# Optimization experiments

Measured on AMD Instinct MI355X. Metric: run time of the kernel, lower is better.

## Reference

```python
import jax, jax.numpy as jnp
import numpy as np

H = 256          # h_dim
SEQ_LEN = 10     # max history length
B = 2048         # number of queries with non-empty history
N = 327680       # total flattened neighbors across all (query, timestep) segments
NUM_SEG = B * SEQ_LEN
NUM_ENT = 20000
NUM_REL = 200


def setup_inputs() -> dict:
    key = jax.random.key(0)
    ks = jax.random.split(key, 9)
    s = jax.random.randint(ks[0], (B,), 0, NUM_ENT)
    r = jax.random.randint(ks[1], (B,), 0, NUM_REL)
    nbr_ids = jax.random.randint(ks[2], (N,), 0, NUM_ENT)
    seg_ids = jnp.sort(jax.random.randint(ks[3], (N,), 0, NUM_SEG))
    ent_embeds = jax.random.normal(ks[4], (NUM_ENT, H), dtype=jnp.float32)
    rel_embeds = jax.random.normal(ks[5], (NUM_REL, H), dtype=jnp.float32)
    W_attn = jax.random.normal(ks[6], (3 * H, H), dtype=jnp.float32) * 0.05
    b_attn = jax.random.normal(ks[7], (H,), dtype=jnp.float32) * 0.05
    v_s = jax.random.normal(ks[8], (H, 1), dtype=jnp.float32) * 0.05
    return {"s": s, "r": r, "nbr_ids": nbr_ids, "seg_ids": seg_ids,
            "ent_embeds": ent_embeds, "rel_embeds": rel_embeds,
            "W_attn": W_attn, "b_attn": b_attn, "v_s": v_s}


def reference(s, r, nbr_ids, seg_ids, ent_embeds, rel_embeds, W_attn, b_attn, v_s):
    # Per-neighbor gathers. Each neighbor belongs to segment seg = q*SEQ_LEN + t.
    q = seg_ids // SEQ_LEN                              # query index per neighbor [N]
    em = ent_embeds[nbr_ids]                            # [N, H] neighbor embeddings
    s_emb = ent_embeds[s]                               # [B, H]
    r_emb = rel_embeds[r]                               # [B, H]
    ss = s_emb[q]                                       # [N, H]
    rr = r_emb[q]                                       # [N, H]
    # Score: tanh(Linear(3H -> H)) @ v_s  -> scalar per neighbor
    x = jnp.concatenate([em, ss, rr], axis=1)           # [N, 3H]
    scores = (jnp.tanh(x @ W_attn + b_attn) @ v_s)[:, 0]  # [N]
    # Segment softmax over neighbors within each (query, timestep) segment.
    m = jax.ops.segment_max(scores, seg_ids, num_segments=NUM_SEG)  # [S]
    e = jnp.exp(scores - m[seg_ids])                    # [N]
    denom = jax.ops.segment_sum(e, seg_ids, num_segments=NUM_SEG)   # [S]
    w = e / denom[seg_ids]                              # [N]
    # Weighted sum of neighbor embeddings per segment (scatter-reduce).
    agg = jax.ops.segment_sum(w[:, None] * em, seg_ids, num_segments=NUM_SEG)  # [S, H]
    counts = jax.ops.segment_sum(jnp.ones_like(scores), seg_ids, num_segments=NUM_SEG)
    mask = (counts > 0).astype(em.dtype).reshape(B, SEQ_LEN, 1)     # present timesteps
    agg = agg.reshape(B, SEQ_LEN, H)
    ss_t = jnp.broadcast_to(s_emb[:, None, :], (B, SEQ_LEN, H))
    rr_t = jnp.broadcast_to(r_emb[:, None, :], (B, SEQ_LEN, H))
    # Padded [B, SEQ_LEN, 3H] sequence tensor (rows for empty segments are zero,
    # matching the torch code's zero-initialized padded tensor). Dropout p=0.0.
    out = jnp.concatenate([agg, ss_t, rr_t], axis=2) * mask
    return out
```

## Files before the change

kernel.cpp:

```cpp
#include <hip/hip_runtime.h>
#include <hip/hip_bf16.h>

#define H 256
#define SEQ 10
#define C2LOG2E 2.8853900817779268f
#define LOG2E 1.4426950408889634f

typedef __attribute__((ext_vector_type(8))) short bf16x8;
typedef __attribute__((ext_vector_type(4))) float f32x4;

__device__ __forceinline__ unsigned short f2bf(float x) {
    union { float f; unsigned u; } v; v.f = x;
    unsigned r = v.u + 0x7fff + ((v.u >> 16) & 1);
    return (unsigned short)(r >> 16);
}
__device__ __forceinline__ float bf2f(unsigned short b) {
    union { unsigned u; float f; } v; v.u = ((unsigned)b) << 16;
    return v.f;
}
__device__ __forceinline__ float fexp2(float x) {
    return __builtin_amdgcn_exp2f(x);
}

__global__ void prep_kernel(const float* __restrict__ W,
                            unsigned short* __restrict__ Wt,
                            const int* __restrict__ seg_ids,
                            int* __restrict__ seg_start,
                            int nWt, int n, int num_seg) {
    if ((int)blockIdx.x < nWt) {
        int idx = blockIdx.x * 256 + threadIdx.x;
        if (idx >= H * 3 * H) return;
        int nn = idx / (3 * H), k = idx % (3 * H);
        Wt[idx] = f2bf(C2LOG2E * W[k * H + nn]);
    } else {
        int j = (blockIdx.x - nWt) * 256 + threadIdx.x;
        if (j >= n) return;
        int cur = seg_ids[j];
        int prev = (j == 0) ? -1 : seg_ids[j - 1];
        for (int s2 = prev + 1; s2 <= cur; s2++) seg_start[s2] = j;
        if (j == n - 1)
            for (int s2 = cur + 1; s2 <= num_seg; s2++) seg_start[s2] = n;
    }
}

__global__ void gemm_bf16_kernel(const float* __restrict__ entf,
                                 const int* __restrict__ sidx,
                                 const int* __restrict__ ridx,
                                 const float* __restrict__ rel,
                                 const unsigned short* __restrict__ Wt,
                                 const float* __restrict__ bias,
                                 unsigned short* __restrict__ comb,
                                 float* __restrict__ Eq,
                                 int nEntBlk, int M0, int M1) {
    __shared__ unsigned short As[64][40];
    bool isEnt = (int)blockIdx.x < nEntBlk;
    int m0 = (isEnt ? blockIdx.x : (blockIdx.x - nEntBlk)) * 64;
    int M = isEnt ? M0 : M1;
    int K = isEnt ? H : 2 * H;
    int k0 = isEnt ? 0 : H;

    int t = threadIdx.x;
    int sr = t >> 2;
    int sc = (t & 3) * 8;
    int wave = t >> 6, lane = t & 63;
    int lr = lane & 15, lg = lane >> 4;

    f32x4 acc[4][4];
#pragma unroll
    for (int i = 0; i < 4; i++)
#pragma unroll
        for (int jn = 0; jn < 4; jn++) acc[i][jn] = (f32x4){0.f, 0.f, 0.f, 0.f};

    const unsigned short* bp[4];
#pragma unroll
    for (int bn = 0; bn < 4; bn++)
        bp[bn] = Wt + (size_t)(wave * 64 + bn * 16 + lr) * (3 * H) + k0 + lg * 8;

    for (int kk = 0; kk < K; kk += 32) {
        bf16x8 av = {};
        int gm = m0 + sr;
        if (gm < M) {
            const float* src;
            if (isEnt) {
                src = entf + (size_t)gm * H + kk + sc;
            } else {
                int k = kk + sc;
                src = (k < H) ? (entf + (size_t)sidx[gm] * H + k)
                              : (rel + (size_t)ridx[gm] * H + (k - H));
            }
            float4 f0 = *reinterpret_cast<const float4*>(src);
            float4 f1 = *reinterpret_cast<const float4*>(src + 4);
            av[0] = (short)f2bf(f0.x); av[1] = (short)f2bf(f0.y);
            av[2] = (short)f2bf(f0.z); av[3] = (short)f2bf(f0.w);
            av[4] = (short)f2bf(f1.x); av[5] = (short)f2bf(f1.y);
            av[6] = (short)f2bf(f1.z); av[7] = (short)f2bf(f1.w);
            if (isEnt)
                *reinterpret_cast<bf16x8*>(comb + (size_t)gm * 512 + 256 + kk + sc) = av;
        }
        *reinterpret_cast<bf16x8*>(&As[sr][sc]) = av;

        bf16x8 bfr[4];
#pragma unroll
        for (int bn = 0; bn < 4; bn++)
            bfr[bn] = *reinterpret_cast<const bf16x8*>(bp[bn] + kk);

        __syncthreads();
        bf16x8 afr[4];
#pragma unroll
        for (int am = 0; am < 4; am++)
            afr[am] = *reinterpret_cast<const bf16x8*>(&As[am * 16 + lr][lg * 8]);
#pragma unroll
        for (int am = 0; am < 4; am++)
#pragma unroll
            for (int bn = 0; bn < 4; bn++)
                acc[am][bn] = __builtin_amdgcn_mfma_f32_16x16x32_bf16(
                    afr[am], bfr[bn], acc[am][bn], 0, 0, 0);
        __syncthreads();
    }

#pragma unroll
    for (int bn = 0; bn < 4; bn++) {
        int col = wave * 64 + bn * 16 + lr;
        float bv = isEnt ? 0.f : C2LOG2E * bias[col];
#pragma unroll
        for (int am = 0; am < 4; am++) {
#pragma unroll
            for (int rr = 0; rr < 4; rr++) {
                int row = m0 + am * 16 + lg * 4 + rr;
                if (row < M) {
                    float ex = fexp2(acc[am][bn][rr] + bv);
                    if (isEnt)
                        comb[(size_t)row * 512 + col] = f2bf(ex);
                    else
                        Eq[(size_t)row * H + col] = ex;
                }
            }
        }
    }
}

__global__ void __launch_bounds__(128)
fused_agg_kernel(const int* __restrict__ nbr_ids,
                 const int* __restrict__ seg_start,
                 const unsigned short* __restrict__ comb,
                 const float* __restrict__ Eq,
                 const float* __restrict__ v_s,
                 const float* __restrict__ ent_embeds,
                 const float* __restrict__ rel_embeds,
                 const int* __restrict__ s,
                 const int* __restrict__ r,
                 float* __restrict__ out, int num_seg) {
    int seg = blockIdx.x * 2 + (threadIdx.x >> 6);
    if (seg >= num_seg) return;
    int lane = threadIdx.x & 63;
    int g = lane >> 4, li = lane & 15;
    int cb = li * 16;
    int c4 = lane * 4;
    int b = seg / SEQ;
    int start = seg_start[seg], end = seg_start[seg + 1];
    float* orow = out + (size_t)seg * (3 * H);

    if (start == end) {
        float4 z = {0.f, 0.f, 0.f, 0.f};
        *reinterpret_cast<float4*>(orow + c4) = z;
        *reinterpret_cast<float4*>(orow + H + c4) = z;
        *reinterpret_cast<float4*>(orow + 2 * H + c4) = z;
        return;
    }

    float4 ssv = *reinterpret_cast<const float4*>(ent_embeds + (size_t)s[b] * H + c4);
    float4 rrv = *reinterpret_cast<const float4*>(rel_embeds + (size_t)r[b] * H + c4);

    float vm2[16];
    float vsum = 0.f;
    {
        const float4* vp = reinterpret_cast<const float4*>(v_s + cb);
#pragma unroll
        for (int k = 0; k < 4; k++) {
            float4 tv = vp[k];
            vm2[4 * k + 0] = -2.f * tv.x; vm2[4 * k + 1] = -2.f * tv.y;
            vm2[4 * k + 2] = -2.f * tv.z; vm2[4 * k + 3] = -2.f * tv.w;
            vsum += tv.x + tv.y + tv.z + tv.w;
        }
    }

    float qv[16];
    {
        const float4* qp = reinterpret_cast<const float4*>(Eq + (size_t)b * H + cb);
#pragma unroll
        for (int k = 0; k < 4; k++) {
            float4 tq = qp[k];
            qv[4 * k + 0] = tq.x; qv[4 * k + 1] = tq.y;
            qv[4 * k + 2] = tq.z; qv[4 * k + 3] = tq.w;
        }
    }

    float acc[16];
#pragma unroll
    for (int k = 0; k < 16; k++) acc[k] = 0.f;
    float lpart = 0.f;

    int cc = end - start;
    int nitm = (cc + 3) >> 2;

    bf16x8 p0 = {}, p1 = {}, e0 = {}, e1 = {};
    if (g < cc) {
        const unsigned short* row = comb + (size_t)nbr_ids[start + g] * 512 + cb;
        p0 = *reinterpret_cast<const bf16x8*>(row);
        p1 = *reinterpret_cast<const bf16x8*>(row + 8);
        e0 = *reinterpret_cast<const bf16x8*>(row + 256);
        e1 = *reinterpret_cast<const bf16x8*>(row + 264);
    }

    for (int ji = 0; ji < nitm; ji++) {
        bf16x8 p0n = {}, p1n = {}, e0n = {}, e1n = {};
        int jn = 4 * (ji + 1) + g;
        if (jn < cc) {
            const unsigned short* rown = comb + (size_t)nbr_ids[start + jn] * 512 + cb;
            p0n = *reinterpret_cast<const bf16x8*>(rown);
            p1n = *reinterpret_cast<const bf16x8*>(rown + 8);
            e0n = *reinterpret_cast<const bf16x8*>(rown + 256);
            e1n = *reinterpret_cast<const bf16x8*>(rown + 264);
        }

        float sa = 0.f, sb = 0.f;
#pragma unroll
        for (int k = 0; k < 8; k += 2) {
            float a0 = fmaf(bf2f((unsigned short)p0[k]), qv[k], 1.f);
            float a1 = fmaf(bf2f((unsigned short)p1[k]), qv[8 + k], 1.f);
            float num = vm2[k] * a1;
            num = fmaf(vm2[8 + k], a0, num);
            sa = fmaf(num, __builtin_amdgcn_rcpf(a0 * a1), sa);
            float b0 = fmaf(bf2f((unsigned short)p0[k + 1]), qv[k + 1], 1.f);
            float b1 = fmaf(bf2f((unsigned short)p1[k + 1]), qv[9 + k], 1.f);
            float numb = vm2[k + 1] * b1;
            numb = fmaf(vm2[9 + k], b0, numb);
            sb = fmaf(numb, __builtin_amdgcn_rcpf(b0 * b1), sb);
        }
        float s16 = sa + sb + vsum;
        s16 += __shfl_xor(s16, 1);
        s16 += __shfl_xor(s16, 2);
        s16 += __shfl_xor(s16, 4);
        s16 += __shfl_xor(s16, 8);
        float e = fexp2(s16 * LOG2E);
        e = (4 * ji + g < cc) ? e : 0.f;
        lpart += e;
#pragma unroll
        for (int k = 0; k < 8; k++) {
            acc[k] = fmaf(e, bf2f((unsigned short)e0[k]), acc[k]);
            acc[8 + k] = fmaf(e, bf2f((unsigned short)e1[k]), acc[8 + k]);
        }
        p0 = p0n; p1 = p1n; e0 = e0n; e1 = e1n;
    }

    lpart += __shfl_xor(lpart, 16);
    lpart += __shfl_xor(lpart, 32);
#pragma unroll
    for (int k = 0; k < 16; k++) {
        acc[k] += __shfl_xor(acc[k], 16);
        acc[k] += __shfl_xor(acc[k], 32);
    }
    float invl = 1.f / lpart;

    float4 o;
#pragma unroll
    for (int k = 0; k < 4; k++) {
        float v0 = acc[k], v1 = acc[4 + k], v2 = acc[8 + k], v3 = acc[12 + k];
        float pick = (g == 0) ? v0 : (g == 1) ? v1 : (g == 2) ? v2 : v3;
        if (k == 0) o.x = pick * invl;
        else if (k == 1) o.y = pick * invl;
        else if (k == 2) o.z = pick * invl;
        else o.w = pick * invl;
    }
    *reinterpret_cast<float4*>(orow + cb + 4 * g) = o;
    *reinterpret_cast<float4*>(orow + H + c4) = ssv;
    *reinterpret_cast<float4*>(orow + 2 * H + c4) = rrv;
}

extern "C" void kernel_launch(void* const* d_in, const int* in_sizes, int n_in,
                              void* d_out, int out_size, void* d_ws, size_t ws_size,
                              hipStream_t stream) {
    const int* s = (const int*)d_in[0];
    const int* r = (const int*)d_in[1];
    const int* nbr_ids = (const int*)d_in[2];
    const int* seg_ids = (const int*)d_in[3];
    const float* ent_embeds = (const float*)d_in[4];
    const float* rel_embeds = (const float*)d_in[5];
    const float* W_attn = (const float*)d_in[6];
    const float* b_attn = (const float*)d_in[7];
    const float* v_s = (const float*)d_in[8];
    float* out = (float*)d_out;

    int B = in_sizes[0];
    int N = in_sizes[2];
    int num_ent = in_sizes[4] / H;
    int num_seg = B * SEQ;

    char* ws = (char*)d_ws;
    unsigned short* comb = (unsigned short*)ws;
    unsigned short* Wt = comb + (size_t)num_ent * 512;
    float* Eq = (float*)(Wt + (size_t)H * 3 * H);
    int* seg_start = (int*)(Eq + (size_t)B * H);

    int nWt = (H * 3 * H + 255) / 256;
    int nSeg = (N + 255) / 256;
    prep_kernel<<<nWt + nSeg, 256, 0, stream>>>(W_attn, Wt, seg_ids, seg_start,
                                                nWt, N, num_seg);

    int nEntBlk = (num_ent + 63) / 64;
    int nQBlk = B / 64;
    gemm_bf16_kernel<<<nEntBlk + nQBlk, 256, 0, stream>>>(
        ent_embeds, s, r, rel_embeds, Wt, b_attn, comb, Eq,
        nEntBlk, num_ent, B);

    fused_agg_kernel<<<(num_seg + 1) / 2, 128, 0, stream>>>(
        nbr_ids, seg_start, comb, Eq, v_s,
        ent_embeds, rel_embeds, s, r, out, num_seg);
}
```

Measured before the change: 92.41 us.

## Deepen neighbor prefetch to three stages and use reduce-scatter for final accumulation

The neighbor loop now keeps three rows per lane in flight instead of one, processing an unrolled group of three per iteration and refilling each slot right after use, so more gather latency is hidden. LOG2E is folded into v_s and vsum, which removes one multiply before exp2. The final cross-group accumulator reduction is a two-step reduce-scatter with fewer shuffles instead of a full all-reduce followed by a select. The deeper prefetch costs more vector registers, which may lower occupancy.

```diff
diff --git a/kernel.cpp b/kernel.cpp
--- a/kernel.cpp
+++ b/kernel.cpp
@@ -178,9 +178,9 @@
 #pragma unroll
         for (int k = 0; k < 4; k++) {
             float4 tv = vp[k];
-            vm2[4 * k + 0] = -2.f * tv.x; vm2[4 * k + 1] = -2.f * tv.y;
-            vm2[4 * k + 2] = -2.f * tv.z; vm2[4 * k + 3] = -2.f * tv.w;
-            vsum += tv.x + tv.y + tv.z + tv.w;
+            vm2[4 * k + 0] = -2.f * LOG2E * tv.x; vm2[4 * k + 1] = -2.f * LOG2E * tv.y;
+            vm2[4 * k + 2] = -2.f * LOG2E * tv.z; vm2[4 * k + 3] = -2.f * LOG2E * tv.w;
+            vsum += LOG2E * (tv.x + tv.y + tv.z + tv.w);
         }
     }
 
@@ -203,74 +203,86 @@
     int cc = end - start;
     int nitm = (cc + 3) >> 2;
 
-    bf16x8 p0 = {}, p1 = {}, e0 = {}, e1 = {};
-    if (g < cc) {
-        const unsigned short* row = comb + (size_t)nbr_ids[start + g] * 512 + cb;
-        p0 = *reinterpret_cast<const bf16x8*>(row);
-        p1 = *reinterpret_cast<const bf16x8*>(row + 8);
-        e0 = *reinterpret_cast<const bf16x8*>(row + 256);
-        e1 = *reinterpret_cast<const bf16x8*>(row + 264);
-    }
-
-    for (int ji = 0; ji < nitm; ji++) {
-        bf16x8 p0n = {}, p1n = {}, e0n = {}, e1n = {};
-        int jn = 4 * (ji + 1) + g;
-        if (jn < cc) {
-            const unsigned short* rown = comb + (size_t)nbr_ids[start + jn] * 512 + cb;
-            p0n = *reinterpret_cast<const bf16x8*>(rown);
-            p1n = *reinterpret_cast<const bf16x8*>(rown + 8);
-            e0n = *reinterpret_cast<const bf16x8*>(rown + 256);
-            e1n = *reinterpret_cast<const bf16x8*>(rown + 264);
-        }
-
-        float sa = 0.f, sb = 0.f;
-#pragma unroll
-        for (int k = 0; k < 8; k += 2) {
-            float a0 = fmaf(bf2f((unsigned short)p0[k]), qv[k], 1.f);
-            float a1 = fmaf(bf2f((unsigned short)p1[k]), qv[8 + k], 1.f);
-            float num = vm2[k] * a1;
-            num = fmaf(vm2[8 + k], a0, num);
-            sa = fmaf(num, __builtin_amdgcn_rcpf(a0 * a1), sa);
-            float b0 = fmaf(bf2f((unsigned short)p0[k + 1]), qv[k + 1], 1.f);
-            float b1 = fmaf(bf2f((unsigned short)p1[k + 1]), qv[9 + k], 1.f);
-            float numb = vm2[k + 1] * b1;
-            numb = fmaf(vm2[9 + k], b0, numb);
-            sb = fmaf(numb, __builtin_amdgcn_rcpf(b0 * b1), sb);
-        }
-        float s16 = sa + sb + vsum;
-        s16 += __shfl_xor(s16, 1);
-        s16 += __shfl_xor(s16, 2);
-        s16 += __shfl_xor(s16, 4);
-        s16 += __shfl_xor(s16, 8);
-        float e = fexp2(s16 * LOG2E);
-        e = (4 * ji + g < cc) ? e : 0.f;
-        lpart += e;
-#pragma unroll
-        for (int k = 0; k < 8; k++) {
-            acc[k] = fmaf(e, bf2f((unsigned short)e0[k]), acc[k]);
-            acc[8 + k] = fmaf(e, bf2f((unsigned short)e1[k]), acc[8 + k]);
-        }
-        p0 = p0n; p1 = p1n; e0 = e0n; e1 = e1n;
+    bf16x8 bp0[3], bp1[3], be0[3], be1[3];
+#pragma unroll
+    for (int u = 0; u < 3; u++) { bp0[u] = {}; bp1[u] = {}; be0[u] = {}; be1[u] = {}; }
+#pragma unroll
+    for (int u = 0; u < 3; u++) {
+        int j = 4 * u + g;
+        if (j < cc) {
+            const unsigned short* row = comb + (size_t)nbr_ids[start + j] * 512 + cb;
+            bp0[u] = *reinterpret_cast<const bf16x8*>(row);
+            bp1[u] = *reinterpret_cast<const bf16x8*>(row + 8);
+            be0[u] = *reinterpret_cast<const bf16x8*>(row + 256);
+            be1[u] = *reinterpret_cast<const bf16x8*>(row + 264);
+        }
+    }
+
+    for (int ji = 0; ji < nitm; ji += 3) {
+#pragma unroll
+        for (int u = 0; u < 3; u++) {
+            float sa = 0.f, sb = 0.f;
+#pragma unroll
+            for (int k = 0; k < 8; k += 2) {
+                float a0 = fmaf(bf2f((unsigned short)bp0[u][k]), qv[k], 1.f);
+                float a1 = fmaf(bf2f((unsigned short)bp1[u][k]), qv[8 + k], 1.f);
+                float num = vm2[k] * a1;
+                num = fmaf(vm2[8 + k], a0, num);
+                sa = fmaf(num, __builtin_amdgcn_rcpf(a0 * a1), sa);
+                float b0 = fmaf(bf2f((unsigned short)bp0[u][k + 1]), qv[k + 1], 1.f);
+                float b1 = fmaf(bf2f((unsigned short)bp1[u][k + 1]), qv[9 + k], 1.f);
+                float numb = vm2[k + 1] * b1;
+                numb = fmaf(vm2[9 + k], b0, numb);
+                sb = fmaf(numb, __builtin_amdgcn_rcpf(b0 * b1), sb);
+            }
+            float s16 = sa + sb + vsum;
+            s16 += __shfl_xor(s16, 1);
+            s16 += __shfl_xor(s16, 2);
+            s16 += __shfl_xor(s16, 4);
+            s16 += __shfl_xor(s16, 8);
+            float e = fexp2(s16);
+            e = (4 * (ji + u) + g < cc) ? e : 0.f;
+            lpart += e;
+#pragma unroll
+            for (int k = 0; k < 8; k++) {
+                acc[k] = fmaf(e, bf2f((unsigned short)be0[u][k]), acc[k]);
+                acc[8 + k] = fmaf(e, bf2f((unsigned short)be1[u][k]), acc[8 + k]);
+            }
+            int jn = 4 * (ji + u + 3) + g;
+            if (jn < cc) {
+                const unsigned short* rown = comb + (size_t)nbr_ids[start + jn] * 512 + cb;
+                bp0[u] = *reinterpret_cast<const bf16x8*>(rown);
+                bp1[u] = *reinterpret_cast<const bf16x8*>(rown + 8);
+                be0[u] = *reinterpret_cast<const bf16x8*>(rown + 256);
+                be1[u] = *reinterpret_cast<const bf16x8*>(rown + 264);
+            }
+        }
     }
 
     lpart += __shfl_xor(lpart, 16);
     lpart += __shfl_xor(lpart, 32);
-#pragma unroll
-    for (int k = 0; k < 16; k++) {
-        acc[k] += __shfl_xor(acc[k], 16);
-        acc[k] += __shfl_xor(acc[k], 32);
-    }
     float invl = 1.f / lpart;
 
+    int gb0 = g & 1, gb1 = g >> 1;
+    float t1[8];
+#pragma unroll
+    for (int j = 0; j < 8; j++) {
+        int sl0 = (j < 4) ? j : 4 + j;
+        int sl1 = sl0 + 4;
+        float mine = gb0 ? acc[sl1] : acc[sl0];
+        float opp  = gb0 ? acc[sl0] : acc[sl1];
+        t1[j] = mine + __shfl_xor(opp, 16);
+    }
     float4 o;
 #pragma unroll
-    for (int k = 0; k < 4; k++) {
-        float v0 = acc[k], v1 = acc[4 + k], v2 = acc[8 + k], v3 = acc[12 + k];
-        float pick = (g == 0) ? v0 : (g == 1) ? v1 : (g == 2) ? v2 : v3;
-        if (k == 0) o.x = pick * invl;
-        else if (k == 1) o.y = pick * invl;
-        else if (k == 2) o.z = pick * invl;
-        else o.w = pick * invl;
+    for (int j = 0; j < 4; j++) {
+        float mine = gb1 ? t1[4 + j] : t1[j];
+        float opp  = gb1 ? t1[j] : t1[4 + j];
+        float fin = (mine + __shfl_xor(opp, 32)) * invl;
+        if (j == 0) o.x = fin;
+        else if (j == 1) o.y = fin;
+        else if (j == 2) o.z = fin;
+        else o.w = fin;
     }
     *reinterpret_cast<float4*>(orow + cb + 4 * g) = o;
     *reinterpret_cast<float4*>(orow + H + c4) = ssv;
```

New measurement: 103.1 us. 1.12x slower.

## Persistent grid-stride agg kernel, move seg_start build into GEMM launch, cheaper reductions

Applied to the files above, without the earlier changes.

The aggregation kernel becomes persistent. It uses 256-thread blocks and a fixed 2560-block grid, and each wave strides over segments, so the v_s setup is loaded once per wave. The seg_start construction moves from the prep kernel into extra blocks of the GEMM launch, which shrinks the small Wt-transpose kernel. LOG2E is folded into v_s to remove a multiply per neighbor. The cross-group accumulator reduction becomes a two-step butterfly that halves the shuffle count. Risks are load imbalance from the fixed grid and higher register pressure.

```diff
diff --git a/kernel.cpp b/kernel.cpp
--- a/kernel.cpp
+++ b/kernel.cpp
@@ -23,24 +23,11 @@
 }
 
 __global__ void prep_kernel(const float* __restrict__ W,
-                            unsigned short* __restrict__ Wt,
-                            const int* __restrict__ seg_ids,
-                            int* __restrict__ seg_start,
-                            int nWt, int n, int num_seg) {
-    if ((int)blockIdx.x < nWt) {
-        int idx = blockIdx.x * 256 + threadIdx.x;
-        if (idx >= H * 3 * H) return;
-        int nn = idx / (3 * H), k = idx % (3 * H);
-        Wt[idx] = f2bf(C2LOG2E * W[k * H + nn]);
-    } else {
-        int j = (blockIdx.x - nWt) * 256 + threadIdx.x;
-        if (j >= n) return;
-        int cur = seg_ids[j];
-        int prev = (j == 0) ? -1 : seg_ids[j - 1];
-        for (int s2 = prev + 1; s2 <= cur; s2++) seg_start[s2] = j;
-        if (j == n - 1)
-            for (int s2 = cur + 1; s2 <= num_seg; s2++) seg_start[s2] = n;
-    }
+                            unsigned short* __restrict__ Wt) {
+    int idx = blockIdx.x * 256 + threadIdx.x;
+    if (idx >= H * 3 * H) return;
+    int nn = idx / (3 * H), k = idx % (3 * H);
+    Wt[idx] = f2bf(C2LOG2E * W[k * H + nn]);
 }
 
 __global__ void gemm_bf16_kernel(const float* __restrict__ entf,
@@ -51,10 +38,25 @@
                                  const float* __restrict__ bias,
                                  unsigned short* __restrict__ comb,
                                  float* __restrict__ Eq,
-                                 int nEntBlk, int M0, int M1) {
+                                 const int* __restrict__ seg_ids,
+                                 int* __restrict__ seg_start,
+                                 int n, int num_seg,
+                                 int nEntBlk, int nQBlk, int M0, int M1) {
+    int bid = blockIdx.x;
+    if (bid >= nEntBlk + nQBlk) {
+        int j = (bid - nEntBlk - nQBlk) * 256 + threadIdx.x;
+        if (j >= n) return;
+        int cur = seg_ids[j];
+        int prev = (j == 0) ? -1 : seg_ids[j - 1];
+        for (int s2 = prev + 1; s2 <= cur; s2++) seg_start[s2] = j;
+        if (j == n - 1)
+            for (int s2 = cur + 1; s2 <= num_seg; s2++) seg_start[s2] = n;
+        return;
+    }
+
     __shared__ unsigned short As[64][40];
-    bool isEnt = (int)blockIdx.x < nEntBlk;
-    int m0 = (isEnt ? blockIdx.x : (blockIdx.x - nEntBlk)) * 64;
+    bool isEnt = bid < nEntBlk;
+    int m0 = (isEnt ? bid : (bid - nEntBlk)) * 64;
     int M = isEnt ? M0 : M1;
     int K = isEnt ? H : 2 * H;
     int k0 = isEnt ? 0 : H;
@@ -139,7 +141,7 @@
     }
 }
 
-__global__ void __launch_bounds__(128)
+__global__ void __launch_bounds__(256)
 fused_agg_kernel(const int* __restrict__ nbr_ids,
                  const int* __restrict__ seg_start,
                  const unsigned short* __restrict__ comb,
@@ -150,26 +152,12 @@
                  const int* __restrict__ s,
                  const int* __restrict__ r,
                  float* __restrict__ out, int num_seg) {
-    int seg = blockIdx.x * 2 + (threadIdx.x >> 6);
-    if (seg >= num_seg) return;
+    int w = threadIdx.x >> 6;
     int lane = threadIdx.x & 63;
     int g = lane >> 4, li = lane & 15;
     int cb = li * 16;
     int c4 = lane * 4;
-    int b = seg / SEQ;
-    int start = seg_start[seg], end = seg_start[seg + 1];
-    float* orow = out + (size_t)seg * (3 * H);
-
-    if (start == end) {
-        float4 z = {0.f, 0.f, 0.f, 0.f};
-        *reinterpret_cast<float4*>(orow + c4) = z;
-        *reinterpret_cast<float4*>(orow + H + c4) = z;
-        *reinterpret_cast<float4*>(orow + 2 * H + c4) = z;
-        return;
-    }
-
-    float4 ssv = *reinterpret_cast<const float4*>(ent_embeds + (size_t)s[b] * H + c4);
-    float4 rrv = *reinterpret_cast<const float4*>(rel_embeds + (size_t)r[b] * H + c4);
+    int nwtot = gridDim.x * 4;
 
     float vm2[16];
     float vsum = 0.f;
@@ -178,103 +166,126 @@
 #pragma unroll
         for (int k = 0; k < 4; k++) {
             float4 tv = vp[k];
-            vm2[4 * k + 0] = -2.f * tv.x; vm2[4 * k + 1] = -2.f * tv.y;
-            vm2[4 * k + 2] = -2.f * tv.z; vm2[4 * k + 3] = -2.f * tv.w;
-            vsum += tv.x + tv.y + tv.z + tv.w;
-        }
-    }
-
-    float qv[16];
-    {
-        const float4* qp = reinterpret_cast<const float4*>(Eq + (size_t)b * H + cb);
-#pragma unroll
-        for (int k = 0; k < 4; k++) {
-            float4 tq = qp[k];
-            qv[4 * k + 0] = tq.x; qv[4 * k + 1] = tq.y;
-            qv[4 * k + 2] = tq.z; qv[4 * k + 3] = tq.w;
-        }
-    }
-
-    float acc[16];
-#pragma unroll
-    for (int k = 0; k < 16; k++) acc[k] = 0.f;
-    float lpart = 0.f;
-
-    int cc = end - start;
-    int nitm = (cc + 3) >> 2;
-
-    bf16x8 p0 = {}, p1 = {}, e0 = {}, e1 = {};
-    if (g < cc) {
-        const unsigned short* row = comb + (size_t)nbr_ids[start + g] * 512 + cb;
-        p0 = *reinterpret_cast<const bf16x8*>(row);
-        p1 = *reinterpret_cast<const bf16x8*>(row + 8);
-        e0 = *reinterpret_cast<const bf16x8*>(row + 256);
-        e1 = *reinterpret_cast<const bf16x8*>(row + 264);
-    }
-
-    for (int ji = 0; ji < nitm; ji++) {
-        bf16x8 p0n = {}, p1n = {}, e0n = {}, e1n = {};
-        int jn = 4 * (ji + 1) + g;
-        if (jn < cc) {
-            const unsigned short* rown = comb + (size_t)nbr_ids[start + jn] * 512 + cb;
-            p0n = *reinterpret_cast<const bf16x8*>(rown);
-            p1n = *reinterpret_cast<const bf16x8*>(rown + 8);
-            e0n = *reinterpret_cast<const bf16x8*>(rown + 256);
-            e1n = *reinterpret_cast<const bf16x8*>(rown + 264);
-        }
-
-        float sa = 0.f, sb = 0.f;
-#pragma unroll
-        for (int k = 0; k < 8; k += 2) {
-            float a0 = fmaf(bf2f((unsigned short)p0[k]), qv[k], 1.f);
-            float a1 = fmaf(bf2f((unsigned short)p1[k]), qv[8 + k], 1.f);
-            float num = vm2[k] * a1;
-            num = fmaf(vm2[8 + k], a0, num);
-            sa = fmaf(num, __builtin_amdgcn_rcpf(a0 * a1), sa);
-            float b0 = fmaf(bf2f((unsigned short)p0[k + 1]), qv[k + 1], 1.f);
-            float b1 = fmaf(bf2f((unsigned short)p1[k + 1]), qv[9 + k], 1.f);
-            float numb = vm2[k + 1] * b1;
-            numb = fmaf(vm2[9 + k], b0, numb);
-            sb = fmaf(numb, __builtin_amdgcn_rcpf(b0 * b1), sb);
-        }
-        float s16 = sa + sb + vsum;
-        s16 += __shfl_xor(s16, 1);
-        s16 += __shfl_xor(s16, 2);
-        s16 += __shfl_xor(s16, 4);
-        s16 += __shfl_xor(s16, 8);
-        float e = fexp2(s16 * LOG2E);
-        e = (4 * ji + g < cc) ? e : 0.f;
-        lpart += e;
-#pragma unroll
-        for (int k = 0; k < 8; k++) {
-            acc[k] = fmaf(e, bf2f((unsigned short)e0[k]), acc[k]);
-            acc[8 + k] = fmaf(e, bf2f((unsigned short)e1[k]), acc[8 + k]);
-        }
-        p0 = p0n; p1 = p1n; e0 = e0n; e1 = e1n;
-    }
-
-    lpart += __shfl_xor(lpart, 16);
-    lpart += __shfl_xor(lpart, 32);
-#pragma unroll
-    for (int k = 0; k < 16; k++) {
-        acc[k] += __shfl_xor(acc[k], 16);
-        acc[k] += __shfl_xor(acc[k], 32);
-    }
-    float invl = 1.f / lpart;
-
-    float4 o;
-#pragma unroll
-    for (int k = 0; k < 4; k++) {
-        float v0 = acc[k], v1 = acc[4 + k], v2 = acc[8 + k], v3 = acc[12 + k];
-        float pick = (g == 0) ? v0 : (g == 1) ? v1 : (g == 2) ? v2 : v3;
-        if (k == 0) o.x = pick * invl;
-        else if (k == 1) o.y = pick * invl;
-        else if (k == 2) o.z = pick * invl;
-        else o.w = pick * invl;
-    }
-    *reinterpret_cast<float4*>(orow + cb + 4 * g) = o;
-    *reinterpret_cast<float4*>(orow + H + c4) = ssv;
-    *reinterpret_cast<float4*>(orow + 2 * H + c4) = rrv;
+            vm2[4 * k + 0] = -2.f * LOG2E * tv.x; vm2[4 * k + 1] = -2.f * LOG2E * tv.y;
+            vm2[4 * k + 2] = -2.f * LOG2E * tv.z; vm2[4 * k + 3] = -2.f * LOG2E * tv.w;
+            vsum += LOG2E * (tv.x + tv.y + tv.z + tv.w);
+        }
+    }
+
+    for (int seg = blockIdx.x * 4 + w; seg < num_seg; seg += nwtot) {
+        int start = seg_start[seg], end = seg_start[seg + 1];
+        int b = seg / SEQ;
+        float* orow = out + (size_t)seg * (3 * H);
+
+        if (start == end) {
+            float4 z = {0.f, 0.f, 0.f, 0.f};
+            *reinterpret_cast<float4*>(orow + c4) = z;
+            *reinterpret_cast<float4*>(orow + H + c4) = z;
+            *reinterpret_cast<float4*>(orow + 2 * H + c4) = z;
+            continue;
+        }
+
+        float4 ssv = *reinterpret_cast<const float4*>(ent_embeds + (size_t)s[b] * H + c4);
+        float4 rrv = *reinterpret_cast<const float4*>(rel_embeds + (size_t)r[b] * H + c4);
+
+        float qv[16];
+        {
+            const float4* qp = reinterpret_cast<const float4*>(Eq + (size_t)b * H + cb);
+#pragma unroll
+            for (int k = 0; k < 4; k++) {
+                float4 tq = qp[k];
+                qv[4 * k + 0] = tq.x; qv[4 * k + 1] = tq.y;
+                qv[4 * k + 2] = tq.z; qv[4 * k + 3] = tq.w;
+            }
+        }
+
+        float acc[16];
+#pragma unroll
+        for (int k = 0; k < 16; k++) acc[k] = 0.f;
+        float lpart = 0.f;
+
+        int cc = end - start;
+        int nitm = (cc + 3) >> 2;
+
+        bf16x8 p0 = {}, p1 = {}, e0 = {}, e1 = {};
+        if (g < cc) {
+            const unsigned short* row = comb + (size_t)nbr_ids[start + g] * 512 + cb;
+            p0 = *reinterpret_cast<const bf16x8*>(row);
+            p1 = *reinterpret_cast<const bf16x8*>(row + 8);
+            e0 = *reinterpret_cast<const bf16x8*>(row + 256);
+            e1 = *reinterpret_cast<const bf16x8*>(row + 264);
+        }
+
+        for (int ji = 0; ji < nitm; ji++) {
+            bf16x8 p0n = {}, p1n = {}, e0n = {}, e1n = {};
+            int jn = 4 * (ji + 1) + g;
+            if (jn < cc) {
+                const unsigned short* rown = comb + (size_t)nbr_ids[start + jn] * 512 + cb;
+                p0n = *reinterpret_cast<const bf16x8*>(rown);
+                p1n = *reinterpret_cast<const bf16x8*>(rown + 8);
+                e0n = *reinterpret_cast<const bf16x8*>(rown + 256);
+                e1n = *reinterpret_cast<const bf16x8*>(rown + 264);
+            }
+
+            float sa = 0.f, sb = 0.f;
+#pragma unroll
+            for (int k = 0; k < 8; k += 2) {
+                float a0 = fmaf(bf2f((unsigned short)p0[k]), qv[k], 1.f);
+                float a1 = fmaf(bf2f((unsigned short)p1[k]), qv[8 + k], 1.f);
+                float num = vm2[k] * a1;
+                num = fmaf(vm2[8 + k], a0, num);
+                sa = fmaf(num, __builtin_amdgcn_rcpf(a0 * a1), sa);
+                float b0 = fmaf(bf2f((unsigned short)p0[k + 1]), qv[k + 1], 1.f);
+                float b1 = fmaf(bf2f((unsigned short)p1[k + 1]), qv[9 + k], 1.f);
+                float numb = vm2[k + 1] * b1;
+                numb = fmaf(vm2[9 + k], b0, numb);
+                sb = fmaf(numb, __builtin_amdgcn_rcpf(b0 * b1), sb);
+            }
+            float s16 = sa + sb + vsum;
+            s16 += __shfl_xor(s16, 1);
+            s16 += __shfl_xor(s16, 2);
+            s16 += __shfl_xor(s16, 4);
+            s16 += __shfl_xor(s16, 8);
+            float e = fexp2(s16);
+            e = (4 * ji + g < cc) ? e : 0.f;
+            lpart += e;
+#pragma unroll
+            for (int k = 0; k < 8; k++) {
+                acc[k] = fmaf(e, bf2f((unsigned short)e0[k]), acc[k]);
+                acc[8 + k] = fmaf(e, bf2f((unsigned short)e1[k]), acc[8 + k]);
+            }
+            p0 = p0n; p1 = p1n; e0 = e0n; e1 = e1n;
+        }
+
+        lpart += __shfl_xor(lpart, 16);
+        lpart += __shfl_xor(lpart, 32);
+        float invl = 1.f / lpart;
+
+        int gb0 = g & 1, gb1 = g >> 1;
+        float t1[8];
+#pragma unroll
+        for (int j = 0; j < 8; j++) {
+            int sl0 = (j < 4) ? j : 4 + j;
+            int sl1 = sl0 + 4;
+            float mine = gb0 ? acc[sl1] : acc[sl0];
+            float opp  = gb0 ? acc[sl0] : acc[sl1];
+            t1[j] = mine + __shfl_xor(opp, 16);
+        }
+        float4 o;
+#pragma unroll
+        for (int j = 0; j < 4; j++) {
+            float mine = gb1 ? t1[4 + j] : t1[j];
+            float opp  = gb1 ? t1[j] : t1[4 + j];
+            float fin = (mine + __shfl_xor(opp, 32)) * invl;
+            if (j == 0) o.x = fin;
+            else if (j == 1) o.y = fin;
+            else if (j == 2) o.z = fin;
+            else o.w = fin;
+        }
+        *reinterpret_cast<float4*>(orow + cb + 4 * g) = o;
+        *reinterpret_cast<float4*>(orow + H + c4) = ssv;
+        *reinterpret_cast<float4*>(orow + 2 * H + c4) = rrv;
+    }
 }
 
 extern "C" void kernel_launch(void* const* d_in, const int* in_sizes, int n_in,
@@ -303,17 +314,16 @@
     int* seg_start = (int*)(Eq + (size_t)B * H);
 
     int nWt = (H * 3 * H + 255) / 256;
-    int nSeg = (N + 255) / 256;
-    prep_kernel<<<nWt + nSeg, 256, 0, stream>>>(W_attn, Wt, seg_ids, seg_start,
-                                                nWt, N, num_seg);
+    prep_kernel<<<nWt, 256, 0, stream>>>(W_attn, Wt);
 
     int nEntBlk = (num_ent + 63) / 64;
     int nQBlk = B / 64;
-    gemm_bf16_kernel<<<nEntBlk + nQBlk, 256, 0, stream>>>(
+    int nSegBlk = (N + 255) / 256;
+    gemm_bf16_kernel<<<nEntBlk + nQBlk + nSegBlk, 256, 0, stream>>>(
         ent_embeds, s, r, rel_embeds, Wt, b_attn, comb, Eq,
-        nEntBlk, num_ent, B);
-
-    fused_agg_kernel<<<(num_seg + 1) / 2, 128, 0, stream>>>(
+        seg_ids, seg_start, N, num_seg, nEntBlk, nQBlk, num_ent, B);
+
+    fused_agg_kernel<<<2560, 256, 0, stream>>>(
         nbr_ids, seg_start, comb, Eq, v_s,
         ent_embeds, rel_embeds, s, r, out, num_seg);
 }
```

New measurement: 109.9 us. 1.19x slower.
